# Kernel tuning notes

Hardware: AMD Instinct MI355X
Metric: run time of the kernel (lower is better)

## Reference

```python
import jax, jax.numpy as jnp
from jax import lax
import numpy as np

WINDOW_SIZE = 11
K1 = 0.01
K2 = 0.03
EPS = 1e-06


def _box_filter(x, k):
    """Depthwise uniform box filter with SAME (zero) padding, matching F.conv2d(..., groups=C)."""
    c = x.shape[1]
    kernel = jnp.full((c, 1, k, k), 1.0 / (k * k), dtype=x.dtype)  # [C,1,k,k]
    pad = k // 2
    return lax.conv_general_dilated(
        x, kernel,
        window_strides=(1, 1),
        padding=[(pad, pad), (pad, pad)],
        dimension_numbers=("NCHW", "OIHW", "NCHW"),
        feature_group_count=c,
    )


def setup_inputs() -> dict:
    key = jax.random.key(0)
    k1, k2 = jax.random.split(key)
    shape = (32, 3, 512, 512)
    pred = jax.random.uniform(k1, shape, dtype=jnp.float32)
    target = jax.random.uniform(k2, shape, dtype=jnp.float32)
    return {"pred": pred, "target": target}


def reference(pred, target):
    k = WINDOW_SIZE
    mu_p = _box_filter(pred, k)
    mu_t = _box_filter(target, k)
    sigma_p = _box_filter(pred * pred, k) - mu_p * mu_p
    sigma_t = _box_filter(target * target, k) - mu_t * mu_t
    sigma_x = _box_filter(pred * target, k) - mu_p * mu_t
    sigma_p = jnp.maximum(sigma_p, 0.0)
    sigma_t = jnp.maximum(sigma_t, 0.0)

    # per (batch, channel) dynamic range over spatial dims
    dyn_max = jnp.max(jnp.maximum(pred, target), axis=(-2, -1), keepdims=True)
    dyn_min = jnp.min(jnp.minimum(pred, target), axis=(-2, -1), keepdims=True)
    data_range = jnp.maximum(dyn_max - dyn_min, EPS)
    c1 = (K1 * data_range) ** 2
    c2 = (K2 * data_range) ** 2

    numerator = (2.0 * mu_p * mu_t + c1) * (2.0 * sigma_x + c2)
    denominator = (mu_p * mu_p + mu_t * mu_t + c1) * (sigma_p + sigma_t + c2)
    ssim_map = numerator / (denominator + EPS)
    loss_map = jnp.maximum((1.0 - ssim_map) * 0.5, 0.0)
    return jnp.mean(loss_map)
```

## Files before the change

kernel.cpp:

```cpp
#include <hip/hip_runtime.h>

constexpr int Wd = 512;
constexpr int PLANE = 512 * 512;

typedef float v2f __attribute__((ext_vector_type(2)));

__global__ __launch_bounds__(256) void minmax_part(const float* __restrict__ pred,
                                                   const float* __restrict__ targ,
                                                   float* __restrict__ pmx,
                                                   float* __restrict__ pmn) {
    int bx = blockIdx.x;
    int plane = bx >> 3, seg = bx & 7;
    size_t base = (size_t)plane * PLANE + (size_t)seg * 32768;
    const float4* p4 = reinterpret_cast<const float4*>(pred + base);
    const float4* t4 = reinterpret_cast<const float4*>(targ + base);
    float mx = -3.0e38f, mn = 3.0e38f;
    for (int i = threadIdx.x; i < 8192; i += 256) {
        float4 a = p4[i], b = t4[i];
        mx = fmaxf(mx, fmaxf(fmaxf(fmaxf(a.x, b.x), fmaxf(a.y, b.y)),
                             fmaxf(fmaxf(a.z, b.z), fmaxf(a.w, b.w))));
        mn = fminf(mn, fminf(fminf(fminf(a.x, b.x), fminf(a.y, b.y)),
                             fminf(fminf(a.z, b.z), fminf(a.w, b.w))));
    }
    #pragma unroll
    for (int off = 32; off; off >>= 1) {
        mx = fmaxf(mx, __shfl_down(mx, off));
        mn = fminf(mn, __shfl_down(mn, off));
    }
    __shared__ float smx[4], smn[4];
    int wid = threadIdx.x >> 6, lane = threadIdx.x & 63;
    if (lane == 0) { smx[wid] = mx; smn[wid] = mn; }
    __syncthreads();
    if (threadIdx.x == 0) {
        pmx[bx] = fmaxf(fmaxf(smx[0], smx[1]), fmaxf(smx[2], smx[3]));
        pmn[bx] = fminf(fminf(smn[0], smn[1]), fminf(smn[2], smn[3]));
    }
}

__global__ void minmax_fin(const float* __restrict__ pmx, const float* __restrict__ pmn,
                           float* __restrict__ c1s, float* __restrict__ c2s, int planes) {
    int p = blockIdx.x * blockDim.x + threadIdx.x;
    if (p < planes) {
        float mx = -3.0e38f, mn = 3.0e38f;
        for (int s = 0; s < 8; ++s) {
            mx = fmaxf(mx, pmx[p * 8 + s]);
            mn = fminf(mn, pmn[p * 8 + s]);
        }
        float dr = fmaxf(mx - mn, 1e-6f);
        c1s[p] = 1.4641f * dr * dr;
        c2s[p] = 13.1769f * dr * dr;
    }
}

__global__ __launch_bounds__(128) void ssim_main(const float* __restrict__ pred,
                                                 const float* __restrict__ targ,
                                                 const float* __restrict__ c1s,
                                                 const float* __restrict__ c2s,
                                                 float* __restrict__ parts) {
    __shared__ float red[2];
    int bx = blockIdx.x;
    int plane = bx >> 3, tile = bx & 7;
    int wid = threadIdx.x >> 6, c = threadIdx.x & 63;
    const float c1 = c1s[plane], c2 = c2s[plane];
    const v2f c1v = {c1, c1}, c2v = {c2, c2};
    const v2f k121 = {121.0f, 121.0f};
    const float* Pg = pred + (size_t)plane * PLANE;
    const float* Tg = targ + (size_t)plane * PLANE;
    int r0 = tile * 64 + wid * 32;
    const bool lane0 = (c == 0), lane63 = (c == 63);

    v2f vsP[4], vsT[4], vsPP[4], vsTT[4], vsPT[4];
    #pragma unroll
    for (int j = 0; j < 4; ++j) {
        vsP[j] = 0; vsT[j] = 0; vsPP[j] = 0; vsTT[j] = 0; vsPT[j] = 0;
    }

    struct RowData { float4 a0, a1, b0, b1; };

    auto load_row = [&](int r) -> RowData {
        RowData d;
        if ((unsigned)r < 512u) {
            const float4* prow = reinterpret_cast<const float4*>(Pg + (size_t)r * Wd);
            const float4* trow = reinterpret_cast<const float4*>(Tg + (size_t)r * Wd);
            d.a0 = prow[2 * c]; d.a1 = prow[2 * c + 1];
            d.b0 = trow[2 * c]; d.b1 = trow[2 * c + 1];
        } else {
            d.a0 = d.a1 = d.b0 = d.b1 = make_float4(0, 0, 0, 0);
        }
        return d;
    };

    auto acc_data = [&](const RowData& d, bool add) {
        v2f pa[4] = {{d.a0.x, d.a0.y}, {d.a0.z, d.a0.w}, {d.a1.x, d.a1.y}, {d.a1.z, d.a1.w}};
        v2f tb[4] = {{d.b0.x, d.b0.y}, {d.b0.z, d.b0.w}, {d.b1.x, d.b1.y}, {d.b1.z, d.b1.w}};
        #pragma unroll
        for (int j = 0; j < 4; ++j) {
            if (add) {
                vsP[j]  += pa[j];
                vsT[j]  += tb[j];
                vsPP[j] += pa[j] * pa[j];
                vsTT[j] += tb[j] * tb[j];
                vsPT[j] += pa[j] * tb[j];
            } else {
                vsP[j]  -= pa[j];
                vsT[j]  -= tb[j];
                vsPP[j] -= pa[j] * pa[j];
                vsTT[j] -= tb[j] * tb[j];
                vsPT[j] -= pa[j] * tb[j];
            }
        }
    };

    auto hsum = [&](const v2f v[4], v2f H[4]) {
        float P0 = v[0].x;
        float P1 = P0 + v[0].y;
        float P2 = P1 + v[1].x;
        float P3 = P2 + v[1].y;
        float P4 = P3 + v[2].x;
        float P5 = P4 + v[2].y;
        float P6 = P5 + v[3].x;
        float T  = P6 + v[3].y;
        float Tm  = __shfl_up(T, 1);
        float Pm2 = __shfl_up(P2, 1);
        float Pm3 = __shfl_up(P3, 1);
        float Pm4 = __shfl_up(P4, 1);
        float Pm5 = __shfl_up(P5, 1);
        float Pm6 = __shfl_up(P6, 1);
        if (lane0) { Tm = 0; Pm2 = 0; Pm3 = 0; Pm4 = 0; Pm5 = 0; Pm6 = 0; }
        float Pp0 = __shfl_down(P0, 1);
        float Pp1 = __shfl_down(P1, 1);
        float Pp2 = __shfl_down(P2, 1);
        float Pp3 = __shfl_down(P3, 1);
        float Pp4 = __shfl_down(P4, 1);
        if (lane63) { Pp0 = 0; Pp1 = 0; Pp2 = 0; Pp3 = 0; Pp4 = 0; }
        H[0].x = (Tm - Pm2) + P5;
        H[0].y = (Tm - Pm3) + P6;
        H[1].x = (Tm - Pm4) + T;
        H[1].y = (Tm - Pm5) + (T + Pp0);
        H[2].x = (Tm - Pm6) + (T + Pp1);
        H[2].y = T + Pp2;
        H[3].x = (T - P0) + Pp3;
        H[3].y = (T - P1) + Pp4;
    };

    v2f lsum2 = {0.0f, 0.0f};

    auto body = [&](int it, const RowData& E, const RowData& Lv, RowData& En, RowData& Ln) {
        En = load_row(r0 + it + 6);
        Ln = load_row(r0 + it - 4);

        acc_data(E, true);

        v2f H[5][4];
        hsum(vsP,  H[0]);
        hsum(vsT,  H[1]);
        hsum(vsPP, H[2]);
        hsum(vsTT, H[3]);
        hsum(vsPT, H[4]);

        #pragma unroll
        for (int j = 0; j < 4; ++j) {
            v2f A = H[0][j], B = H[1][j];
            v2f AB = A * B, A2 = A * A, B2 = B * B;
            v2f t4 = k121 * H[4][j] - AB;
            v2f num = (2.0f * AB + c1v) * (2.0f * t4 + c2v);
            v2f sp = k121 * H[2][j] - A2;
            v2f st = k121 * H[3][j] - B2;
            sp.x = fmaxf(sp.x, 0.0f); sp.y = fmaxf(sp.y, 0.0f);
            st.x = fmaxf(st.x, 0.0f); st.y = fmaxf(st.y, 0.0f);
            v2f den = (A2 + B2 + c1v) * (sp + st + c2v);
            float s0 = __fdividef(num.x, den.x + 214.358881f);
            float s1 = __fdividef(num.y, den.y + 214.358881f);
            v2f loss = {fmaxf((1.0f - s0) * 0.5f, 0.0f),
                        fmaxf((1.0f - s1) * 0.5f, 0.0f)};
            lsum2 += loss;
        }
        acc_data(Lv, false);
    };

    {
        RowData D0 = load_row(r0 - 5), D1 = load_row(r0 - 4), D2 = load_row(r0 - 3),
                D3 = load_row(r0 - 2), D4 = load_row(r0 - 1);
        acc_data(D0, true); acc_data(D1, true); acc_data(D2, true);
        acc_data(D3, true); acc_data(D4, true);
        RowData D5 = load_row(r0 + 0), D6 = load_row(r0 + 1), D7 = load_row(r0 + 2),
                D8 = load_row(r0 + 3), D9 = load_row(r0 + 4);
        acc_data(D5, true); acc_data(D6, true); acc_data(D7, true);
        acc_data(D8, true); acc_data(D9, true);
    }

    RowData E0 = load_row(r0 + 5);
    RowData L0 = load_row(r0 - 5);
    RowData E1, L1;

    #pragma unroll 1
    for (int it = 0; it < 32; it += 2) {
        body(it,     E0, L0, E1, L1);
        body(it + 1, E1, L1, E0, L0);
    }

    float lsum = lsum2.x + lsum2.y;
    #pragma unroll
    for (int off = 32; off; off >>= 1) lsum += __shfl_down(lsum, off);
    if (c == 0) red[wid] = lsum;
    __syncthreads();
    if (threadIdx.x == 0) parts[bx] = red[0] + red[1];
}

__global__ void finish(const float* __restrict__ parts, float* __restrict__ out,
                       int n, float invN) {
    float s = 0.0f;
    for (int i = threadIdx.x; i < n; i += 256) s += parts[i];
    #pragma unroll
    for (int off = 32; off; off >>= 1) s += __shfl_down(s, off);
    __shared__ float sw[4];
    int wid = threadIdx.x >> 6, lane = threadIdx.x & 63;
    if (lane == 0) sw[wid] = s;
    __syncthreads();
    if (threadIdx.x == 0) out[0] = ((sw[0] + sw[1]) + (sw[2] + sw[3])) * invN;
}

extern "C" void kernel_launch(void* const* d_in, const int* in_sizes, int n_in,
                              void* d_out, int out_size, void* d_ws, size_t ws_size,
                              hipStream_t stream) {
    const float* pred = (const float*)d_in[0];
    const float* targ = (const float*)d_in[1];
    float* out = (float*)d_out;
    int planes = in_sizes[0] / PLANE;
    int G = planes * 8;

    float* ws   = (float*)d_ws;
    float* pmx  = ws;
    float* pmn  = ws + G;
    float* c1s  = ws + 2 * G;
    float* c2s  = ws + 2 * G + planes;
    float* prts = ws + 2 * G + 2 * planes;

    minmax_part<<<G, 256, 0, stream>>>(pred, targ, pmx, pmn);
    minmax_fin<<<(planes + 127) / 128, 128, 0, stream>>>(pmx, pmn, c1s, c2s, planes);
    ssim_main<<<G, 128, 0, stream>>>(pred, targ, c1s, c2s, prts);
    float invN = 1.0f / ((float)planes * (float)PLANE);
    finish<<<1, 256, 0, stream>>>(prts, out, G, invN);
}
```

Baseline: 117.8 us.

## Split each wave's 32-row sliding window into two interleaved 16-row chains

Result: slower. 159.7 us (+35.6%).

```diff
diff --git a/kernel.cpp b/kernel.cpp
--- a/kernel.cpp
+++ b/kernel.cpp
@@ -66,16 +66,14 @@
     const v2f k121 = {121.0f, 121.0f};
     const float* Pg = pred + (size_t)plane * PLANE;
     const float* Tg = targ + (size_t)plane * PLANE;
-    int r0 = tile * 64 + wid * 32;
+    int wr0 = tile * 64 + wid * 32;
     const bool lane0 = (c == 0), lane63 = (c == 63);
 
-    v2f vsP[4], vsT[4], vsPP[4], vsTT[4], vsPT[4];
-    #pragma unroll
-    for (int j = 0; j < 4; ++j) {
-        vsP[j] = 0; vsT[j] = 0; vsPP[j] = 0; vsTT[j] = 0; vsPT[j] = 0;
-    }
-
     struct RowData { float4 a0, a1, b0, b1; };
+    struct Chain {
+        v2f vsP[4], vsT[4], vsPP[4], vsTT[4], vsPT[4];
+        RowData E, L;
+    };
 
     auto load_row = [&](int r) -> RowData {
         RowData d;
@@ -90,23 +88,23 @@
         return d;
     };
 
-    auto acc_data = [&](const RowData& d, bool add) {
+    auto acc_data = [&](Chain& ch, const RowData& d, bool add) {
         v2f pa[4] = {{d.a0.x, d.a0.y}, {d.a0.z, d.a0.w}, {d.a1.x, d.a1.y}, {d.a1.z, d.a1.w}};
         v2f tb[4] = {{d.b0.x, d.b0.y}, {d.b0.z, d.b0.w}, {d.b1.x, d.b1.y}, {d.b1.z, d.b1.w}};
         #pragma unroll
         for (int j = 0; j < 4; ++j) {
             if (add) {
-                vsP[j]  += pa[j];
-                vsT[j]  += tb[j];
-                vsPP[j] += pa[j] * pa[j];
-                vsTT[j] += tb[j] * tb[j];
-                vsPT[j] += pa[j] * tb[j];
+                ch.vsP[j]  += pa[j];
+                ch.vsT[j]  += tb[j];
+                ch.vsPP[j] += pa[j] * pa[j];
+                ch.vsTT[j] += tb[j] * tb[j];
+                ch.vsPT[j] += pa[j] * tb[j];
             } else {
-                vsP[j]  -= pa[j];
-                vsT[j]  -= tb[j];
-                vsPP[j] -= pa[j] * pa[j];
-                vsTT[j] -= tb[j] * tb[j];
-                vsPT[j] -= pa[j] * tb[j];
+                ch.vsP[j]  -= pa[j];
+                ch.vsT[j]  -= tb[j];
+                ch.vsPP[j] -= pa[j] * pa[j];
+                ch.vsTT[j] -= tb[j] * tb[j];
+                ch.vsPT[j] -= pa[j] * tb[j];
             }
         }
     };
@@ -143,21 +141,15 @@
         H[3].y = (T - P1) + Pp4;
     };
 
-    v2f lsum2 = {0.0f, 0.0f};
-
-    auto body = [&](int it, const RowData& E, const RowData& Lv, RowData& En, RowData& Ln) {
-        En = load_row(r0 + it + 6);
-        Ln = load_row(r0 + it - 4);
-
-        acc_data(E, true);
-
+    v2f lsumA = {0.0f, 0.0f}, lsumB = {0.0f, 0.0f};
+
+    auto hepi = [&](Chain& ch, v2f& lsum2) {
         v2f H[5][4];
-        hsum(vsP,  H[0]);
-        hsum(vsT,  H[1]);
-        hsum(vsPP, H[2]);
-        hsum(vsTT, H[3]);
-        hsum(vsPT, H[4]);
-
+        hsum(ch.vsP,  H[0]);
+        hsum(ch.vsT,  H[1]);
+        hsum(ch.vsPP, H[2]);
+        hsum(ch.vsTT, H[3]);
+        hsum(ch.vsPT, H[4]);
         #pragma unroll
         for (int j = 0; j < 4; ++j) {
             v2f A = H[0][j], B = H[1][j];
@@ -175,30 +167,45 @@
                         fmaxf((1.0f - s1) * 0.5f, 0.0f)};
             lsum2 += loss;
         }
-        acc_data(Lv, false);
-    };
-
-    {
+    };
+
+    auto init_chain = [&](Chain& ch, int r0) {
+        #pragma unroll
+        for (int j = 0; j < 4; ++j) {
+            ch.vsP[j] = 0; ch.vsT[j] = 0; ch.vsPP[j] = 0; ch.vsTT[j] = 0; ch.vsPT[j] = 0;
+        }
         RowData D0 = load_row(r0 - 5), D1 = load_row(r0 - 4), D2 = load_row(r0 - 3),
                 D3 = load_row(r0 - 2), D4 = load_row(r0 - 1);
-        acc_data(D0, true); acc_data(D1, true); acc_data(D2, true);
-        acc_data(D3, true); acc_data(D4, true);
+        acc_data(ch, D0, true); acc_data(ch, D1, true); acc_data(ch, D2, true);
+        acc_data(ch, D3, true); acc_data(ch, D4, true);
         RowData D5 = load_row(r0 + 0), D6 = load_row(r0 + 1), D7 = load_row(r0 + 2),
                 D8 = load_row(r0 + 3), D9 = load_row(r0 + 4);
-        acc_data(D5, true); acc_data(D6, true); acc_data(D7, true);
-        acc_data(D8, true); acc_data(D9, true);
-    }
-
-    RowData E0 = load_row(r0 + 5);
-    RowData L0 = load_row(r0 - 5);
-    RowData E1, L1;
+        acc_data(ch, D5, true); acc_data(ch, D6, true); acc_data(ch, D7, true);
+        acc_data(ch, D8, true); acc_data(ch, D9, true);
+        ch.E = load_row(r0 + 5);
+        ch.L = load_row(r0 - 5);
+    };
+
+    const int r0A = wr0, r0B = wr0 + 16;
+    Chain chA, chB;
+    init_chain(chA, r0A);
+    init_chain(chB, r0B);
 
     #pragma unroll 1
-    for (int it = 0; it < 32; it += 2) {
-        body(it,     E0, L0, E1, L1);
-        body(it + 1, E1, L1, E0, L0);
-    }
-
+    for (int it = 0; it < 16; ++it) {
+        acc_data(chA, chA.E, true);
+        chA.E = load_row(r0A + it + 6);
+        acc_data(chB, chB.E, true);
+        chB.E = load_row(r0B + it + 6);
+        hepi(chA, lsumA);
+        acc_data(chA, chA.L, false);
+        chA.L = load_row(r0A + it - 4);
+        hepi(chB, lsumB);
+        acc_data(chB, chB.L, false);
+        chB.L = load_row(r0B + it - 4);
+    }
+
+    v2f lsum2 = lsumA + lsumB;
     float lsum = lsum2.x + lsum2.y;
     #pragma unroll
     for (int off = 32; off; off >>= 1) lsum += __shfl_down(lsum, off);
```
